# Performance work log

Hardware: AMD Instinct MI355X
Metric: run time of the kernel (lower is better)

Reference implementation:

```python
import jax, jax.numpy as jnp
import numpy as np

B, S, E, L, H, FF, CB = 16, 1000, 512, 4, 8, 2048, 4096
DH = E // H

def _ln(x, g, b):
    m = x.mean(-1, keepdims=True)
    v = ((x - m) ** 2).mean(-1, keepdims=True)
    return (x - m) / jnp.sqrt(v + 1e-5) * g + b

def setup_inputs() -> dict:
    key = jax.random.key(0)
    cnt = [0]
    def rn(shape, s=0.02):
        cnt[0] += 1
        return jax.random.normal(jax.random.fold_in(key, cnt[0]), shape, jnp.float32) * s
    inp = {}
    inp['noisy_tokens'] = jax.random.randint(jax.random.fold_in(key, 999), (B, S), 0, CB, dtype=jnp.int32)
    inp['codebook'] = rn((CB, E), 1.0)
    # sinusoidal positional encoding, as in _create_positional_encoding
    pe = np.zeros((S, E), np.float32)
    pos = np.arange(S, dtype=np.float32)[:, None]
    div = np.exp(np.arange(0, E, 2, dtype=np.float32) * (-np.log(10000.0) / E))
    pe[:, 0::2] = np.sin(pos * div)
    pe[:, 1::2] = np.cos(pos * div)
    inp['pos_enc'] = jnp.asarray(pe)[None]  # [1,S,E]
    # transformer encoder layers (stacked over L)
    inp['qkv_w'] = rn((L, 3 * E, E)); inp['qkv_b'] = jnp.zeros((L, 3 * E))
    inp['out_w'] = rn((L, E, E));     inp['out_b'] = jnp.zeros((L, E))
    inp['ln1_g'] = jnp.ones((L, E));  inp['ln1_b'] = jnp.zeros((L, E))
    inp['ln2_g'] = jnp.ones((L, E));  inp['ln2_b'] = jnp.zeros((L, E))
    inp['ff1_w'] = rn((L, FF, E));    inp['ff1_b'] = jnp.zeros((L, FF))
    inp['ff2_w'] = rn((L, E, FF));    inp['ff2_b'] = jnp.zeros((L, E))
    inp['fin_g'] = jnp.ones((E,));    inp['fin_b'] = jnp.zeros((E,))
    # post_process: Linear, LN, GELU, Linear
    inp['pp1_w'] = rn((E, E)); inp['pp1_b'] = jnp.zeros((E,))
    inp['pp_ln_g'] = jnp.ones((E,)); inp['pp_ln_b'] = jnp.zeros((E,))
    inp['pp2_w'] = rn((E, E)); inp['pp2_b'] = jnp.zeros((E,))
    inp['res_w'] = jnp.float32(0.1)
    # feature_to_codebook: Linear, LN, GELU, Linear (codebook_dim == E)
    inp['fc1_w'] = rn((E, E)); inp['fc1_b'] = jnp.zeros((E,))
    inp['fc_ln_g'] = jnp.ones((E,)); inp['fc_ln_b'] = jnp.zeros((E,))
    inp['fc2_w'] = rn((E, E)); inp['fc2_b'] = jnp.zeros((E,))
    return inp

def reference(noisy_tokens, codebook, pos_enc, qkv_w, qkv_b, out_w, out_b,
              ln1_g, ln1_b, ln2_g, ln2_b, ff1_w, ff1_b, ff2_w, ff2_b,
              fin_g, fin_b, pp1_w, pp1_b, pp_ln_g, pp_ln_b, pp2_w, pp2_b,
              res_w, fc1_w, fc1_b, fc_ln_g, fc_ln_b, fc2_w, fc2_b):
    gelu = lambda z: jax.nn.gelu(z, approximate=False)
    # token embedding (codebook_projection is Identity) + positional encoding
    x = codebook[noisy_tokens] + pos_enc            # [B,S,E]
    # pre-norm transformer encoder (dropout=0 / eval)
    y = x
    for l in range(L):
        h = _ln(y, ln1_g[l], ln1_b[l])
        qkv = h @ qkv_w[l].T + qkv_b[l]             # [B,S,3E]
        q, k, v = jnp.split(qkv, 3, axis=-1)
        q = q.reshape(B, S, H, DH); k = k.reshape(B, S, H, DH); v = v.reshape(B, S, H, DH)
        scores = jnp.einsum('bqhd,bkhd->bhqk', q, k) / jnp.sqrt(jnp.float32(DH))
        attn = jax.nn.softmax(scores, axis=-1)
        ctx = jnp.einsum('bhqk,bkhd->bqhd', attn, v).reshape(B, S, E)
        y = y + (ctx @ out_w[l].T + out_b[l])
        h2 = _ln(y, ln2_g[l], ln2_b[l])
        y = y + (gelu(h2 @ ff1_w[l].T + ff1_b[l]) @ ff2_w[l].T + ff2_b[l])
    y = _ln(y, fin_g, fin_b)
    # post_process + residual
    pp = gelu(_ln(y @ pp1_w.T + pp1_b, pp_ln_g, pp_ln_b)) @ pp2_w.T + pp2_b
    enhanced = x + res_w * pp
    # feature_to_codebook
    fc = gelu(_ln(enhanced @ fc1_w.T + fc1_b, fc_ln_g, fc_ln_b)) @ fc2_w.T + fc2_b  # [B,S,E]
    # quantize: nearest neighbour in codebook (cdist + argmin)
    flat = fc.reshape(-1, E)
    d2 = (jnp.sum(flat ** 2, -1, keepdims=True)
          - 2.0 * flat @ codebook.T
          + jnp.sum(codebook ** 2, -1))            # [B*S, CB]
    tokens = jnp.argmin(d2, axis=-1).reshape(B, S)
    return fc, tokens
```

## Files before the change

kernel.cpp:

```cpp
#include <hip/hip_runtime.h>
#include <hip/hip_bf16.h>
#include <math.h>

#define NTOK 16000
#define E    512
#define FFD  2048
#define CBN  4096
#define SEQ  1000
#define NH   8
#define VLD  1008

typedef __hip_bfloat16 bf16;
typedef __attribute__((ext_vector_type(8))) short short8;
typedef __attribute__((ext_vector_type(4))) float f32x4;

__device__ __forceinline__ float gelu_f(float v) {
    return 0.5f * v * (1.0f + erff(v * 0.70710678118654752f));
}

__device__ __forceinline__ void split_store(float v, bf16* hi, bf16* lo, size_t idx) {
    bf16 h = __float2bfloat16(v);
    hi[idx] = h;
    lo[idx] = __float2bfloat16(v - __bfloat162float(h));
}

__device__ __forceinline__ void gll16(const bf16* g, short* l) {
    __builtin_amdgcn_global_load_lds((const __attribute__((address_space(1))) void*)g,
                                     (__attribute__((address_space(3))) void*)l, 16, 0, 0);
}

__device__ __forceinline__ void t2_ins(float v, int c, float& v1, int& c1, float& v2, int& c2) {
    const bool b1 = (v < v1) || (v == v1 && c < c1);
    const bool b2 = (v < v2) || (v == v2 && c < c2);
    if (b1) { v2 = v1; c2 = c1; v1 = v; c1 = c; }
    else if (b2) { v2 = v; c2 = c; }
}

__global__ __launch_bounds__(128) void embed_kernel(const int* __restrict__ tok,
                                                    const float* __restrict__ cb,
                                                    const float* __restrict__ pe,
                                                    float* __restrict__ y) {
    const int row = blockIdx.x;
    const int s = row % SEQ;
    const int t = tok[row];
    const int c = threadIdx.x * 4;
    const float4 cv = *(const float4*)(cb + (size_t)t * E + c);
    const float4 pv = *(const float4*)(pe + (size_t)s * E + c);
    *(float4*)(y + (size_t)row * E + c) =
        make_float4(cv.x + pv.x, cv.y + pv.y, cv.z + pv.z, cv.w + pv.w);
}

__global__ __launch_bounds__(256) void split_w(const float* __restrict__ src, int ld,
                                               int cols_log2, int n,
                                               bf16* __restrict__ hi, bf16* __restrict__ lo) {
    const int i = blockIdx.x * 256 + threadIdx.x;
    if (i >= n) return;
    const int r = i >> cols_log2;
    const int c = i & ((1 << cols_log2) - 1);
    const float v = src[(size_t)r * ld + c];
    split_store(v, hi, lo, i);
}

template<int GELU>
__global__ __launch_bounds__(256) void ln_planes(const float* __restrict__ in,
                                                 bf16* __restrict__ hi, bf16* __restrict__ lo,
                                                 const float* __restrict__ g,
                                                 const float* __restrict__ b) {
    const int lane = threadIdx.x & 63;
    const int row = blockIdx.x * 4 + (threadIdx.x >> 6);
    const float* p = in + (size_t)row * E;
    const float4 v0 = *(const float4*)(p + lane * 4);
    const float4 v1 = *(const float4*)(p + 256 + lane * 4);
    float sum = v0.x + v0.y + v0.z + v0.w + v1.x + v1.y + v1.z + v1.w;
    float sq = v0.x * v0.x + v0.y * v0.y + v0.z * v0.z + v0.w * v0.w
             + v1.x * v1.x + v1.y * v1.y + v1.z * v1.z + v1.w * v1.w;
#pragma unroll
    for (int m = 1; m < 64; m <<= 1) {
        sum += __shfl_xor(sum, m);
        sq += __shfl_xor(sq, m);
    }
    const float mean = sum * (1.0f / 512.0f);
    const float var = sq * (1.0f / 512.0f) - mean * mean;
    const float rstd = rsqrtf(var + 1e-5f);
    const float4 g0 = *(const float4*)(g + lane * 4);
    const float4 g1 = *(const float4*)(g + 256 + lane * 4);
    const float4 b0 = *(const float4*)(b + lane * 4);
    const float4 b1 = *(const float4*)(b + 256 + lane * 4);
    const size_t base = (size_t)row * E;
    float o;
    const float vv0[4] = {v0.x, v0.y, v0.z, v0.w};
    const float gg0[4] = {g0.x, g0.y, g0.z, g0.w};
    const float bb0[4] = {b0.x, b0.y, b0.z, b0.w};
    const float vv1[4] = {v1.x, v1.y, v1.z, v1.w};
    const float gg1[4] = {g1.x, g1.y, g1.z, g1.w};
    const float bb1[4] = {b1.x, b1.y, b1.z, b1.w};
#pragma unroll
    for (int t = 0; t < 4; ++t) {
        o = (vv0[t] - mean) * rstd * gg0[t] + bb0[t];
        if (GELU) o = gelu_f(o);
        split_store(o, hi, lo, base + lane * 4 + t);
        o = (vv1[t] - mean) * rstd * gg1[t] + bb1[t];
        if (GELU) o = gelu_f(o);
        split_store(o, hi, lo, base + 256 + lane * 4 + t);
    }
}

template<int OUT>
__global__ __launch_bounds__(256) void gemm_split(
    const bf16* __restrict__ Ah, const bf16* __restrict__ Al, int lda,
    const bf16* __restrict__ Wh, const bf16* __restrict__ Wl, int ldw,
    const float* __restrict__ bias,
    float* __restrict__ C, int ldc,
    bf16* __restrict__ Ohi, bf16* __restrict__ Olo, int ldp,
    const int* __restrict__ noisy, const float* __restrict__ cb,
    const float* __restrict__ pe, const float* __restrict__ resw,
    int K) {
    __shared__ __align__(16) short SB[2][4][128][32];
    const int tid = threadIdx.x;
    const int rowBase = blockIdx.y * 128;
    const int colBase = blockIdx.x * 128;
    const int wave = tid >> 6, lane = tid & 63;
    const int wm = (wave & 1) * 64, wn = (wave >> 1) * 64;
    const int lm = lane & 15;
    const int psl8 = ((lane >> 4) ^ ((lm >> 1) & 3)) * 8;

    const bf16* src = (wave == 0) ? Ah : (wave == 1) ? Al : (wave == 2) ? Wh : Wl;
    const int sld = (wave < 2) ? lda : ldw;
    const int srb = (wave < 2) ? rowBase : colBase;
    const int sslot = (lane & 3) ^ ((lane >> 3) & 3);
    const bf16* sp = src + (size_t)(srb + (lane >> 2)) * sld + sslot * 8;
    short* lb0 = &SB[0][wave][0][0];
    short* lb1 = &SB[1][wave][0][0];

    f32x4 acc[4][4];
#pragma unroll
    for (int i = 0; i < 4; ++i)
#pragma unroll
        for (int j = 0; j < 4; ++j)
            acc[i][j] = (f32x4){0.f, 0.f, 0.f, 0.f};

    const int nt = K >> 5;
#pragma unroll
    for (int j = 0; j < 8; ++j)
        gll16(sp + (size_t)j * 16 * sld, lb0 + j * 512);
    {
        const bf16* p = sp + 32;
#pragma unroll
        for (int j = 0; j < 8; ++j)
            gll16(p + (size_t)j * 16 * sld, lb1 + j * 512);
    }
    for (int t = 0; t < nt; ++t) {
        const int cur = t & 1;
        if (t + 1 < nt) asm volatile("s_waitcnt vmcnt(8)" ::: "memory");
        else            asm volatile("s_waitcnt vmcnt(0)" ::: "memory");
        __builtin_amdgcn_s_barrier();
        __builtin_amdgcn_sched_barrier(0);
        const short (*P)[128][32] = SB[cur];
        short8 ah[4], al[4], wh[4], wl[4];
#pragma unroll
        for (int i = 0; i < 4; ++i) {
            ah[i] = *(const short8*)&P[0][wm + i * 16 + lm][psl8];
            al[i] = *(const short8*)&P[1][wm + i * 16 + lm][psl8];
            wh[i] = *(const short8*)&P[2][wn + i * 16 + lm][psl8];
            wl[i] = *(const short8*)&P[3][wn + i * 16 + lm][psl8];
        }
#pragma unroll
        for (int i = 0; i < 4; ++i)
#pragma unroll
            for (int j = 0; j < 4; ++j)
                acc[i][j] = __builtin_amdgcn_mfma_f32_16x16x32_bf16(ah[i], wh[j], acc[i][j], 0, 0, 0);
#pragma unroll
        for (int i = 0; i < 4; ++i)
#pragma unroll
            for (int j = 0; j < 4; ++j)
                acc[i][j] = __builtin_amdgcn_mfma_f32_16x16x32_bf16(ah[i], wl[j], acc[i][j], 0, 0, 0);
#pragma unroll
        for (int i = 0; i < 4; ++i)
#pragma unroll
            for (int j = 0; j < 4; ++j)
                acc[i][j] = __builtin_amdgcn_mfma_f32_16x16x32_bf16(al[i], wh[j], acc[i][j], 0, 0, 0);
        __builtin_amdgcn_s_barrier();
        if (t + 2 < nt) {
            short* lb = cur ? lb1 : lb0;
            const bf16* p = sp + (t + 2) * 32;
#pragma unroll
            for (int j = 0; j < 8; ++j)
                gll16(p + (size_t)j * 16 * sld, lb + j * 512);
        }
    }

    float bv[4];
#pragma unroll
    for (int j = 0; j < 4; ++j)
        bv[j] = bias ? bias[colBase + wn + j * 16 + lm] : 0.f;
    float scv = 0.f;
    if (OUT == 3) scv = resw[0];
#pragma unroll
    for (int i = 0; i < 4; ++i) {
#pragma unroll
        for (int reg = 0; reg < 4; ++reg) {
            const int r = rowBase + wm + i * 16 + (lane >> 4) * 4 + reg;
            int tok = 0, srow = 0;
            if (OUT == 3) { tok = noisy[r]; srow = r % SEQ; }
#pragma unroll
            for (int j = 0; j < 4; ++j) {
                const int col = colBase + wn + j * 16 + lm;
                float v = acc[i][j][reg] + bv[j];
                if (OUT == 0) {
                    C[(size_t)r * ldc + col] = v;
                } else if (OUT == 1) {
                    float* cp = C + (size_t)r * ldc + col;
                    *cp = *cp + v;
                } else if (OUT == 2) {
                    v = gelu_f(v);
                    split_store(v, Ohi, Olo, (size_t)r * ldp + col);
                } else if (OUT == 3) {
                    const float xv = cb[(size_t)tok * E + col] + pe[(size_t)srow * E + col];
                    v = xv + scv * v;
                    split_store(v, Ohi, Olo, (size_t)r * ldp + col);
                } else if (OUT == 4) {
                    split_store(v, Ohi, Olo, (size_t)r * ldp + col);
                } else {
                    C[(size_t)r * ldc + col] = v;
                    split_store(v, Ohi, Olo, (size_t)r * ldp + col);
                }
            }
        }
    }
}

__global__ __launch_bounds__(256) void vtrans(const bf16* __restrict__ vh_src,
                                              const bf16* __restrict__ vl_src,
                                              bf16* __restrict__ vth,
                                              bf16* __restrict__ vtl) {
    __shared__ short T[64][72];
    const int tid = threadIdx.x;
    const int st = blockIdx.x;
    const int bh = blockIdx.y;
    const int b = bh >> 3, h = bh & 7;
    const int sr = tid >> 2, dq = (tid & 3) * 16;
    const int s_g = st * 64 + sr;
    const int od = tid >> 3;
    const int osq = (tid & 7) * 8;
#pragma unroll
    for (int p = 0; p < 2; ++p) {
        const short* src = (const short*)(p ? vl_src : vh_src);
        short* dst = (short*)(p ? vtl : vth);
        short8 a0 = {0, 0, 0, 0, 0, 0, 0, 0};
        short8 a1 = {0, 0, 0, 0, 0, 0, 0, 0};
        if (s_g < SEQ) {
            const short* sp = src + (size_t)(b * SEQ + s_g) * 1536 + 1024 + h * 64 + dq;
            a0 = *(const short8*)sp;
            a1 = *(const short8*)(sp + 8);
        }
        __syncthreads();
#pragma unroll
        for (int j = 0; j < 8; ++j) T[dq + j][sr] = a0[j];
#pragma unroll
        for (int j = 0; j < 8; ++j) T[dq + 8 + j][sr] = a1[j];
        __syncthreads();
        const int scol = st * 64 + osq;
        if (scol + 8 <= VLD) {
            const short8 o0 = *(const short8*)&T[od][osq];
            const short8 o1 = *(const short8*)&T[od + 32][osq];
            *(short8*)(dst + (size_t)(bh * 64 + od) * VLD + scol) = o0;
            *(short8*)(dst + (size_t)(bh * 64 + od + 32) * VLD + scol) = o1;
        }
    }
}

__global__ __launch_bounds__(256) void attn_mfma(const bf16* __restrict__ qkh,
                                                 const bf16* __restrict__ qkl,
                                                 const bf16* __restrict__ vth,
                                                 const bf16* __restrict__ vtl,
                                                 bf16* __restrict__ chi,
                                                 bf16* __restrict__ clo) {
    __shared__ short QPs[2][64][72];
    __shared__ short Ks[2][64][72];
    __shared__ short Vs[2][64][72];
    const int tid = threadIdx.x;
    const int qt = blockIdx.x, bh = blockIdx.y;
    const int b = bh >> 3, h = bh & 7;
    const int wave = tid >> 6, lane = tid & 63;
    const int lm = lane & 15, g = lane >> 4, q8 = g * 8;
    const int wq = wave * 16;
    const int r0 = tid >> 2, kq = (tid & 3) * 16;
    const short8 z = {0, 0, 0, 0, 0, 0, 0, 0};

    {
        const int q = qt * 64 + r0;
        short8 a0 = z, a1 = z, b0 = z, b1 = z;
        if (q < SEQ) {
            const size_t base = (size_t)(b * SEQ + q) * 1536 + h * 64 + kq;
            a0 = *(const short8*)((const short*)qkh + base);
            a1 = *(const short8*)((const short*)qkh + base + 8);
            b0 = *(const short8*)((const short*)qkl + base);
            b1 = *(const short8*)((const short*)qkl + base + 8);
        }
        *(short8*)&QPs[0][r0][kq] = a0; *(short8*)&QPs[0][r0][kq + 8] = a1;
        *(short8*)&QPs[1][r0][kq] = b0; *(short8*)&QPs[1][r0][kq + 8] = b1;
    }
    __syncthreads();
    short8 qfh[2], qfl[2];
#pragma unroll
    for (int t = 0; t < 2; ++t) {
        qfh[t] = *(const short8*)&QPs[0][wq + lm][t * 32 + q8];
        qfl[t] = *(const short8*)&QPs[1][wq + lm][t * 32 + q8];
    }

    float m_i[4] = {-3e38f, -3e38f, -3e38f, -3e38f};
    float l_i[4] = {0.f, 0.f, 0.f, 0.f};
    f32x4 o[4];
#pragma unroll
    for (int dt = 0; dt < 4; ++dt) o[dt] = (f32x4){0.f, 0.f, 0.f, 0.f};

    short8 ka0 = z, ka1 = z, kl0 = z, kl1 = z;
    short8 va0 = z, va1 = z, vl0 = z, vl1 = z;
    auto loadKV = [&](int kb2) {
        const int kr = kb2 + r0;
        ka0 = z; ka1 = z; kl0 = z; kl1 = z;
        if (kr < SEQ) {
            const size_t base = (size_t)(b * SEQ + kr) * 1536 + 512 + h * 64 + kq;
            ka0 = *(const short8*)((const short*)qkh + base);
            ka1 = *(const short8*)((const short*)qkh + base + 8);
            kl0 = *(const short8*)((const short*)qkl + base);
            kl1 = *(const short8*)((const short*)qkl + base + 8);
        }
        const size_t vbase = (size_t)(bh * 64 + r0) * VLD + kb2 + kq;
        va0 = z; va1 = z; vl0 = z; vl1 = z;
        if (kb2 + kq + 8 <= VLD) {
            va0 = *(const short8*)((const short*)vth + vbase);
            vl0 = *(const short8*)((const short*)vtl + vbase);
        }
        if (kb2 + kq + 16 <= VLD) {
            va1 = *(const short8*)((const short*)vth + vbase + 8);
            vl1 = *(const short8*)((const short*)vtl + vbase + 8);
        }
    };
    loadKV(0);

    for (int kb = 0; kb < SEQ; kb += 64) {
        __syncthreads();
        {
            *(short8*)&Ks[0][r0][kq] = ka0; *(short8*)&Ks[0][r0][kq + 8] = ka1;
            *(short8*)&Ks[1][r0][kq] = kl0; *(short8*)&Ks[1][r0][kq + 8] = kl1;
            *(short8*)&Vs[0][r0][kq] = va0; *(short8*)&Vs[0][r0][kq + 8] = va1;
            *(short8*)&Vs[1][r0][kq] = vl0; *(short8*)&Vs[1][r0][kq + 8] = vl1;
        }
        __syncthreads();
        if (kb + 64 < SEQ) loadKV(kb + 64);
        f32x4 sac[4];
#pragma unroll
        for (int j = 0; j < 4; ++j) sac[j] = (f32x4){0.f, 0.f, 0.f, 0.f};
#pragma unroll
        for (int t = 0; t < 2; ++t) {
#pragma unroll
            for (int j = 0; j < 4; ++j) {
                const short8 kh = *(const short8*)&Ks[0][j * 16 + lm][t * 32 + q8];
                const short8 kl = *(const short8*)&Ks[1][j * 16 + lm][t * 32 + q8];
                sac[j] = __builtin_amdgcn_mfma_f32_16x16x32_bf16(qfh[t], kh, sac[j], 0, 0, 0);
                sac[j] = __builtin_amdgcn_mfma_f32_16x16x32_bf16(qfh[t], kl, sac[j], 0, 0, 0);
                sac[j] = __builtin_amdgcn_mfma_f32_16x16x32_bf16(qfl[t], kh, sac[j], 0, 0, 0);
            }
        }
        float alpha_v[4];
#pragma unroll
        for (int reg = 0; reg < 4; ++reg) {
            float sv[4];
            float rm = -3e38f;
#pragma unroll
            for (int j = 0; j < 4; ++j) {
                const int kc = kb + j * 16 + lm;
                float s = sac[j][reg] * 0.125f;
                s = (kc < SEQ) ? s : -3e38f;
                sv[j] = s;
                rm = fmaxf(rm, s);
            }
#pragma unroll
            for (int m = 1; m < 16; m <<= 1) rm = fmaxf(rm, __shfl_xor(rm, m));
            const float mn = fmaxf(m_i[reg], rm);
            const float al = expf(m_i[reg] - mn);
            float rs = 0.f;
            const int prow = wq + g * 4 + reg;
#pragma unroll
            for (int j = 0; j < 4; ++j) {
                const float pv = expf(sv[j] - mn);
                rs += pv;
                bf16 phb = __float2bfloat16(pv);
                bf16 plb = __float2bfloat16(pv - __bfloat162float(phb));
                QPs[0][prow][j * 16 + lm] = *reinterpret_cast<short*>(&phb);
                QPs[1][prow][j * 16 + lm] = *reinterpret_cast<short*>(&plb);
            }
#pragma unroll
            for (int m = 1; m < 16; m <<= 1) rs += __shfl_xor(rs, m);
            l_i[reg] = l_i[reg] * al + rs;
            m_i[reg] = mn;
            alpha_v[reg] = al;
        }
        const f32x4 av = {alpha_v[0], alpha_v[1], alpha_v[2], alpha_v[3]};
#pragma unroll
        for (int dt = 0; dt < 4; ++dt) o[dt] *= av;
        __syncthreads();
#pragma unroll
        for (int t = 0; t < 2; ++t) {
            const short8 ph = *(const short8*)&QPs[0][wq + lm][t * 32 + q8];
            const short8 pl = *(const short8*)&QPs[1][wq + lm][t * 32 + q8];
#pragma unroll
            for (int dt = 0; dt < 4; ++dt) {
                const short8 vh = *(const short8*)&Vs[0][dt * 16 + lm][t * 32 + q8];
                const short8 vl = *(const short8*)&Vs[1][dt * 16 + lm][t * 32 + q8];
                o[dt] = __builtin_amdgcn_mfma_f32_16x16x32_bf16(ph, vh, o[dt], 0, 0, 0);
                o[dt] = __builtin_amdgcn_mfma_f32_16x16x32_bf16(ph, vl, o[dt], 0, 0, 0);
                o[dt] = __builtin_amdgcn_mfma_f32_16x16x32_bf16(pl, vh, o[dt], 0, 0, 0);
            }
        }
    }
#pragma unroll
    for (int reg = 0; reg < 4; ++reg) {
        const int q = qt * 64 + wq + g * 4 + reg;
        if (q < SEQ) {
            const float inv = 1.0f / l_i[reg];
#pragma unroll
            for (int dt = 0; dt < 4; ++dt) {
                const size_t idx = (size_t)(b * SEQ + q) * E + h * 64 + dt * 16 + lm;
                split_store(o[dt][reg] * inv, chi, clo, idx);
            }
        }
    }
}

__global__ __launch_bounds__(256) void cbnorm_kernel(const float* __restrict__ cb,
                                                     float* __restrict__ out) {
    const int lane = threadIdx.x & 63;
    const int row = blockIdx.x * 4 + (threadIdx.x >> 6);
    const float* p = cb + (size_t)row * E;
    const float4 v0 = *(const float4*)(p + lane * 4);
    const float4 v1 = *(const float4*)(p + 256 + lane * 4);
    float sq = v0.x * v0.x + v0.y * v0.y + v0.z * v0.z + v0.w * v0.w
             + v1.x * v1.x + v1.y * v1.y + v1.z * v1.z + v1.w * v1.w;
#pragma unroll
    for (int m = 1; m < 64; m <<= 1) sq += __shfl_xor(sq, m);
    if (lane == 0) out[row] = sq;
}

__global__ __launch_bounds__(256, 1) void argmin_mfma(
    const bf16* __restrict__ Ah, const bf16* __restrict__ Al,
    const bf16* __restrict__ Wh, const bf16* __restrict__ Wl,
    const float* __restrict__ cbn, float4* __restrict__ part) {
    __shared__ __align__(16) short Wreg[2][8192];
    const int tid = threadIdx.x;
    const int rowBase = blockIdx.x * 64;
    const int wave = tid >> 6, lane = tid & 63;
    const int lm = lane & 15, g = lane >> 4;
    const int g8 = g * 8;
    const int psl8 = (g ^ ((lm >> 1) & 3)) * 8;
    const int sslot = (lane & 3) ^ ((lane >> 3) & 3);
    const int srow = lane >> 2;
    const int row = rowBase + wave * 16 + lm;

    short8 a_h[16], a_l[16];
#pragma unroll
    for (int c = 0; c < 16; ++c) {
        a_h[c] = *(const short8*)(Ah + (size_t)row * E + c * 32 + g8);
        a_l[c] = *(const short8*)(Al + (size_t)row * E + c * 32 + g8);
    }

    auto stageW = [&](int s) {
        const int ct = s >> 4, k = s & 15;
        const int colB = ct * 128;
        short* dstb = &Wreg[s & 1][0];
#pragma unroll
        for (int e = 0; e < 4; ++e) {
            const int m = wave * 4 + e;
            const int p = m >> 3;
            const int j = m & 7;
            const bf16* srcp = p ? Wl : Wh;
            gll16(srcp + (size_t)(colB + j * 16 + srow) * E + k * 32 + sslot * 8,
                  dstb + ((p * 128 + j * 16) * 32));
        }
    };
    stageW(0);
    stageW(1);

    float rv1[4], rv2[4];
    int rc1[4], rc2[4];
#pragma unroll
    for (int r = 0; r < 4; ++r) {
        rv1[r] = 3e38f; rv2[r] = 3e38f;
        rc1[r] = 0x7fffffff; rc2[r] = 0x7fffffff;
    }
    f32x4 acc[8];
#pragma unroll
    for (int j = 0; j < 8; ++j) acc[j] = (f32x4){0.f, 0.f, 0.f, 0.f};

    for (int ct = 0; ct < 32; ++ct) {
        const int colB = ct * 128;
#pragma unroll
        for (int k = 0; k < 16; ++k) {
            const int s = ct * 16 + k;
            if (s + 1 < 512) asm volatile("s_waitcnt vmcnt(4)" ::: "memory");
            else             asm volatile("s_waitcnt vmcnt(0)" ::: "memory");
            __builtin_amdgcn_s_barrier();
            __builtin_amdgcn_sched_barrier(0);
            const short* B = &Wreg[s & 1][0];
#pragma unroll
            for (int j = 0; j < 8; ++j) {
                const short8 wh = *(const short8*)(B + (j * 16 + lm) * 32 + psl8);
                const short8 wl = *(const short8*)(B + (128 + j * 16 + lm) * 32 + psl8);
                acc[j] = __builtin_amdgcn_mfma_f32_16x16x32_bf16(a_h[k], wh, acc[j], 0, 0, 0);
                acc[j] = __builtin_amdgcn_mfma_f32_16x16x32_bf16(a_h[k], wl, acc[j], 0, 0, 0);
                acc[j] = __builtin_amdgcn_mfma_f32_16x16x32_bf16(a_l[k], wh, acc[j], 0, 0, 0);
            }
            __builtin_amdgcn_s_barrier();
            if (s + 2 < 512) stageW(s + 2);
        }
#pragma unroll
        for (int j = 0; j < 8; ++j) {
            const int col = colB + j * 16 + lm;
            const float nv = cbn[col];
#pragma unroll
            for (int r = 0; r < 4; ++r) {
                const float d = nv - 2.0f * acc[j][r];
                t2_ins(d, col, rv1[r], rc1[r], rv2[r], rc2[r]);
            }
            acc[j] = (f32x4){0.f, 0.f, 0.f, 0.f};
        }
    }

#pragma unroll
    for (int r = 0; r < 4; ++r) {
#pragma unroll
        for (int m = 1; m < 16; m <<= 1) {
            const float w1 = __shfl_xor(rv1[r], m); const int d1 = __shfl_xor(rc1[r], m);
            const float w2 = __shfl_xor(rv2[r], m); const int d2 = __shfl_xor(rc2[r], m);
            t2_ins(w1, d1, rv1[r], rc1[r], rv2[r], rc2[r]);
            t2_ins(w2, d2, rv1[r], rc1[r], rv2[r], rc2[r]);
        }
    }
    if (lm == 0) {
#pragma unroll
        for (int r = 0; r < 4; ++r)
            part[rowBase + wave * 16 + g * 4 + r] =
                make_float4(rv1[r], (float)rc1[r], rv2[r], (float)rc2[r]);
    }
}

__global__ __launch_bounds__(256) void argmin_exact(const float4* __restrict__ part,
                                                    const float* __restrict__ fc,
                                                    const float* __restrict__ cb,
                                                    const float* __restrict__ cbn,
                                                    float* __restrict__ tokf) {
    const int wave = threadIdx.x >> 6, lane = threadIdx.x & 63;
    const int r = blockIdx.x * 4 + wave;
    const float4 p = part[r];
    const int c1 = (int)p.y;
    const int c2 = (int)p.w;
    const float* fr = fc + (size_t)r * E + lane * 8;
    const float* p1 = cb + (size_t)c1 * E + lane * 8;
    const float* p2 = cb + (size_t)c2 * E + lane * 8;
    float d1 = 0.f, d2 = 0.f;
#pragma unroll
    for (int j = 0; j < 8; ++j) {
        const float f = fr[j];
        d1 += f * p1[j];
        d2 += f * p2[j];
    }
#pragma unroll
    for (int m = 1; m < 64; m <<= 1) {
        d1 += __shfl_xor(d1, m);
        d2 += __shfl_xor(d2, m);
    }
    d1 = cbn[c1] - 2.0f * d1;
    d2 = cbn[c2] - 2.0f * d2;
    const int win = ((d1 < d2) || (d1 == d2 && c1 < c2)) ? c1 : c2;
    if (lane == 0) tokf[r] = (float)win;
}

extern "C" void kernel_launch(void* const* d_in, const int* in_sizes, int n_in,
                              void* d_out, int out_size, void* d_ws, size_t ws_size,
                              hipStream_t stream) {
    const int* noisy = (const int*)d_in[0];
    const float* codebook = (const float*)d_in[1];
    const float* pos_enc = (const float*)d_in[2];
    const float* qkv_w = (const float*)d_in[3];
    const float* qkv_b = (const float*)d_in[4];
    const float* out_w = (const float*)d_in[5];
    const float* out_b = (const float*)d_in[6];
    const float* ln1_g = (const float*)d_in[7];
    const float* ln1_b = (const float*)d_in[8];
    const float* ln2_g = (const float*)d_in[9];
    const float* ln2_b = (const float*)d_in[10];
    const float* ff1_w = (const float*)d_in[11];
    const float* ff1_b = (const float*)d_in[12];
    const float* ff2_w = (const float*)d_in[13];
    const float* ff2_b = (const float*)d_in[14];
    const float* fin_g = (const float*)d_in[15];
    const float* fin_b = (const float*)d_in[16];
    const float* pp1_w = (const float*)d_in[17];
    const float* pp1_b = (const float*)d_in[18];
    const float* pp_ln_g = (const float*)d_in[19];
    const float* pp_ln_b = (const float*)d_in[20];
    const float* pp2_w = (const float*)d_in[21];
    const float* pp2_b = (const float*)d_in[22];
    const float* res_w = (const float*)d_in[23];
    const float* fc1_w = (const float*)d_in[24];
    const float* fc1_b = (const float*)d_in[25];
    const float* fc_ln_g = (const float*)d_in[26];
    const float* fc_ln_b = (const float*)d_in[27];
    const float* fc2_w = (const float*)d_in[28];
    const float* fc2_b = (const float*)d_in[29];

    float* ws = (float*)d_ws;
    float* y = ws;
    float* REG = ws + 8192000;
    bf16* qkvh = (bf16*)REG;
    bf16* qkvl = qkvh + 24576000;
    bf16* mid_hi = (bf16*)REG;
    bf16* mid_lo = mid_hi + 16384000;
    float* slotA = REG;
    float* slotB = REG + 8192000;
    bf16* e_hi = (bf16*)slotA;
    bf16* e_lo = e_hi + 8192000;
    bf16* fcp2_hi = (bf16*)(REG + 16384000);
    bf16* fcp2_lo = fcp2_hi + 8192000;
    float* WV = ws + 32768000;
    bf16* vth = (bf16*)WV;
    bf16* vtl = vth + 8192 * VLD;
    bf16* wA_hi = (bf16*)WV;
    bf16* wA_lo = wA_hi + 1048576;
    bf16* wB_hi = wA_lo + 1048576;
    bf16* wB_lo = wB_hi + 1048576;
    bf16* cbh = wB_lo + 1048576;
    bf16* cbl = cbh + 2097152;
    float* cbn = slotB;
    float4* part = (float4*)(slotB + 4096);
    bf16* h_hi = (bf16*)d_out;
    bf16* h_lo = h_hi + 8192000;
    float* tokf = (float*)d_out + 8192000;

    const dim3 blk(256);
    const dim3 g512(4, 125), g1024(8, 125), g1536(12, 125);

    embed_kernel<<<dim3(NTOK), dim3(128), 0, stream>>>(noisy, codebook, pos_enc, y);

    for (int l = 0; l < 4; ++l) {
        ln_planes<0><<<dim3(4000), blk, 0, stream>>>(y, h_hi, h_lo, ln1_g + l * E, ln1_b + l * E);
        split_w<<<dim3(3072), blk, 0, stream>>>(qkv_w + (size_t)l * 1536 * E, E, 9, 1536 * E, wA_hi, wA_lo);
        gemm_split<4><<<g1536, blk, 0, stream>>>(
            h_hi, h_lo, E, wA_hi, wA_lo, E, qkv_b + (size_t)l * 1536,
            nullptr, 0, qkvh, qkvl, 1536, nullptr, nullptr, nullptr, nullptr, E);
        vtrans<<<dim3(16, 128), blk, 0, stream>>>(qkvh, qkvl, vth, vtl);
        attn_mfma<<<dim3(16, 128), blk, 0, stream>>>(qkvh, qkvl, vth, vtl, h_hi, h_lo);
        split_w<<<dim3(1024), blk, 0, stream>>>(out_w + (size_t)l * E * E, E, 9, E * E, wB_hi, wB_lo);
        gemm_split<1><<<g512, blk, 0, stream>>>(
            h_hi, h_lo, E, wB_hi, wB_lo, E, out_b + (size_t)l * E,
            y, E, nullptr, nullptr, 0, nullptr, nullptr, nullptr, nullptr, E);
        ln_planes<0><<<dim3(4000), blk, 0, stream>>>(y, h_hi, h_lo, ln2_g + l * E, ln2_b + l * E);
        split_w<<<dim3(4096), blk, 0, stream>>>(ff1_w + (size_t)l * FFD * E, E, 9, FFD * E, wA_hi, wA_lo);
        split_w<<<dim3(4096), blk, 0, stream>>>(ff2_w + (size_t)l * E * FFD, FFD, 11, E * FFD, wB_hi, wB_lo);
        for (int c = 0; c < 2; ++c) {
            gemm_split<2><<<g1024, blk, 0, stream>>>(
                h_hi, h_lo, E, wA_hi + (size_t)c * 1024 * E, wA_lo + (size_t)c * 1024 * E, E,
                ff1_b + (size_t)l * FFD + c * 1024,
                nullptr, 0, mid_hi, mid_lo, 1024, nullptr, nullptr, nullptr, nullptr, E);
            gemm_split<1><<<g512, blk, 0, stream>>>(
                mid_hi, mid_lo, 1024, wB_hi + c * 1024, wB_lo + c * 1024, FFD,
                (c == 0) ? (ff2_b + (size_t)l * E) : nullptr,
                y, E, nullptr, nullptr, 0, nullptr, nullptr, nullptr, nullptr, 1024);
        }
    }

    ln_planes<0><<<dim3(4000), blk, 0, stream>>>(y, h_hi, h_lo, fin_g, fin_b);
    split_w<<<dim3(1024), blk, 0, stream>>>(pp1_w, E, 9, E * E, wA_hi, wA_lo);
    gemm_split<0><<<g512, blk, 0, stream>>>(
        h_hi, h_lo, E, wA_hi, wA_lo, E, pp1_b,
        slotB, E, nullptr, nullptr, 0, nullptr, nullptr, nullptr, nullptr, E);
    ln_planes<1><<<dim3(4000), blk, 0, stream>>>(slotB, h_hi, h_lo, pp_ln_g, pp_ln_b);
    split_w<<<dim3(1024), blk, 0, stream>>>(pp2_w, E, 9, E * E, wB_hi, wB_lo);
    gemm_split<3><<<g512, blk, 0, stream>>>(
        h_hi, h_lo, E, wB_hi, wB_lo, E, pp2_b,
        nullptr, 0, e_hi, e_lo, E, noisy, codebook, pos_enc, res_w, E);
    split_w<<<dim3(1024), blk, 0, stream>>>(fc1_w, E, 9, E * E, wA_hi, wA_lo);
    gemm_split<0><<<g512, blk, 0, stream>>>(
        e_hi, e_lo, E, wA_hi, wA_lo, E, fc1_b,
        slotB, E, nullptr, nullptr, 0, nullptr, nullptr, nullptr, nullptr, E);
    ln_planes<1><<<dim3(4000), blk, 0, stream>>>(slotB, h_hi, h_lo, fc_ln_g, fc_ln_b);
    split_w<<<dim3(1024), blk, 0, stream>>>(fc2_w, E, 9, E * E, wB_hi, wB_lo);
    gemm_split<5><<<g512, blk, 0, stream>>>(
        h_hi, h_lo, E, wB_hi, wB_lo, E, fc2_b,
        slotA, E, fcp2_hi, fcp2_lo, E, nullptr, nullptr, nullptr, nullptr, E);

    split_w<<<dim3(8192), blk, 0, stream>>>(codebook, E, 9, CBN * E, cbh, cbl);
    cbnorm_kernel<<<dim3(1024), blk, 0, stream>>>(codebook, cbn);
    argmin_mfma<<<dim3(250), blk, 0, stream>>>(fcp2_hi, fcp2_lo, cbh, cbl, cbn, part);
    argmin_exact<<<dim3(4000), blk, 0, stream>>>(part, slotA, codebook, cbn, tokf);
    hipMemcpyAsync(d_out, slotA, (size_t)8192000 * 4, hipMemcpyDeviceToDevice, stream);
}
```

Measured before the change: 3.663 ms.

## Split argmin codebook columns across two wave groups with 512-thread blocks

Doubles the argmin_mfma block to 8 waves. Each row group of 16 rows is now handled by two waves, each covering half of the 128 codebook columns per tile, and the W staging load is split across all 8 waves. The two partial top-2 results per row are merged through shared memory at the end. This is meant to raise wave occupancy and latency hiding in the codebook distance kernel, which runs only 250 blocks. In exchange, every A fragment is now loaded into registers by twice as many waves, and the kernel gains a final shared-memory merge with extra barriers.

```diff
diff --git a/kernel.cpp b/kernel.cpp
--- a/kernel.cpp
+++ b/kernel.cpp
@@ -443,7 +443,7 @@
     if (lane == 0) out[row] = sq;
 }
 
-__global__ __launch_bounds__(256, 1) void argmin_mfma(
+__global__ __launch_bounds__(512) void argmin_mfma(
     const bf16* __restrict__ Ah, const bf16* __restrict__ Al,
     const bf16* __restrict__ Wh, const bf16* __restrict__ Wl,
     const float* __restrict__ cbn, float4* __restrict__ part) {
@@ -451,18 +451,25 @@
     const int tid = threadIdx.x;
     const int rowBase = blockIdx.x * 64;
     const int wave = tid >> 6, lane = tid & 63;
+    const int rowg = wave & 3;
+    const int chalf = wave >> 2;
     const int lm = lane & 15, g = lane >> 4;
     const int g8 = g * 8;
     const int psl8 = (g ^ ((lm >> 1) & 3)) * 8;
     const int sslot = (lane & 3) ^ ((lane >> 3) & 3);
     const int srow = lane >> 2;
-    const int row = rowBase + wave * 16 + lm;
+    const int row = rowBase + rowg * 16 + lm;
 
     short8 a_h[16], a_l[16];
 #pragma unroll
     for (int c = 0; c < 16; ++c) {
         a_h[c] = *(const short8*)(Ah + (size_t)row * E + c * 32 + g8);
         a_l[c] = *(const short8*)(Al + (size_t)row * E + c * 32 + g8);
+    }
+#pragma unroll
+    for (int c = 0; c < 16; ++c) {
+        asm volatile("" : "+v"(a_h[c]));
+        asm volatile("" : "+v"(a_l[c]));
     }
 
     auto stageW = [&](int s) {
@@ -470,8 +477,8 @@
         const int colB = ct * 128;
         short* dstb = &Wreg[s & 1][0];
 #pragma unroll
-        for (int e = 0; e < 4; ++e) {
-            const int m = wave * 4 + e;
+        for (int e = 0; e < 2; ++e) {
+            const int m = wave * 2 + e;
             const int p = m >> 3;
             const int j = m & 7;
             const bf16* srcp = p ? Wl : Wh;
@@ -489,24 +496,25 @@
         rv1[r] = 3e38f; rv2[r] = 3e38f;
         rc1[r] = 0x7fffffff; rc2[r] = 0x7fffffff;
     }
-    f32x4 acc[8];
-#pragma unroll
-    for (int j = 0; j < 8; ++j) acc[j] = (f32x4){0.f, 0.f, 0.f, 0.f};
+    f32x4 acc[4];
+#pragma unroll
+    for (int j = 0; j < 4; ++j) acc[j] = (f32x4){0.f, 0.f, 0.f, 0.f};
 
     for (int ct = 0; ct < 32; ++ct) {
         const int colB = ct * 128;
 #pragma unroll
         for (int k = 0; k < 16; ++k) {
             const int s = ct * 16 + k;
-            if (s + 1 < 512) asm volatile("s_waitcnt vmcnt(4)" ::: "memory");
+            if (s + 1 < 512) asm volatile("s_waitcnt vmcnt(2)" ::: "memory");
             else             asm volatile("s_waitcnt vmcnt(0)" ::: "memory");
             __builtin_amdgcn_s_barrier();
             __builtin_amdgcn_sched_barrier(0);
             const short* B = &Wreg[s & 1][0];
 #pragma unroll
-            for (int j = 0; j < 8; ++j) {
-                const short8 wh = *(const short8*)(B + (j * 16 + lm) * 32 + psl8);
-                const short8 wl = *(const short8*)(B + (128 + j * 16 + lm) * 32 + psl8);
+            for (int j = 0; j < 4; ++j) {
+                const int jj = chalf * 4 + j;
+                const short8 wh = *(const short8*)(B + (jj * 16 + lm) * 32 + psl8);
+                const short8 wl = *(const short8*)(B + (128 + jj * 16 + lm) * 32 + psl8);
                 acc[j] = __builtin_amdgcn_mfma_f32_16x16x32_bf16(a_h[k], wh, acc[j], 0, 0, 0);
                 acc[j] = __builtin_amdgcn_mfma_f32_16x16x32_bf16(a_h[k], wl, acc[j], 0, 0, 0);
                 acc[j] = __builtin_amdgcn_mfma_f32_16x16x32_bf16(a_l[k], wh, acc[j], 0, 0, 0);
@@ -515,8 +523,8 @@
             if (s + 2 < 512) stageW(s + 2);
         }
 #pragma unroll
-        for (int j = 0; j < 8; ++j) {
-            const int col = colB + j * 16 + lm;
+        for (int j = 0; j < 4; ++j) {
+            const int col = colB + (chalf * 4 + j) * 16 + lm;
             const float nv = cbn[col];
 #pragma unroll
             for (int r = 0; r < 4; ++r) {
@@ -537,11 +545,23 @@
             t2_ins(w2, d2, rv1[r], rc1[r], rv2[r], rc2[r]);
         }
     }
+    __syncthreads();
+    float4* mbuf = reinterpret_cast<float4*>(&Wreg[0][0]);
     if (lm == 0) {
 #pragma unroll
         for (int r = 0; r < 4; ++r)
-            part[rowBase + wave * 16 + g * 4 + r] =
+            mbuf[(rowg * 16 + g * 4 + r) * 2 + chalf] =
                 make_float4(rv1[r], (float)rc1[r], rv2[r], (float)rc2[r]);
+    }
+    __syncthreads();
+    if (tid < 64) {
+        const float4 p0 = mbuf[tid * 2 + 0];
+        const float4 p1 = mbuf[tid * 2 + 1];
+        float v1 = p0.x, v2 = p0.z;
+        int c1 = (int)p0.y, c2 = (int)p0.w;
+        t2_ins(p1.x, (int)p1.y, v1, c1, v2, c2);
+        t2_ins(p1.z, (int)p1.w, v1, c1, v2, c2);
+        part[rowBase + tid] = make_float4(v1, (float)c1, v2, (float)c2);
     }
 }
 
@@ -692,7 +712,7 @@
 
     split_w<<<dim3(8192), blk, 0, stream>>>(codebook, E, 9, CBN * E, cbh, cbl);
     cbnorm_kernel<<<dim3(1024), blk, 0, stream>>>(codebook, cbn);
-    argmin_mfma<<<dim3(250), blk, 0, stream>>>(fcp2_hi, fcp2_lo, cbh, cbl, cbn, part);
+    argmin_mfma<<<dim3(250), dim3(512), 0, stream>>>(fcp2_hi, fcp2_lo, cbh, cbl, cbn, part);
     argmin_exact<<<dim3(4000), blk, 0, stream>>>(part, slotA, codebook, cbn, tokf);
     hipMemcpyAsync(d_out, slotA, (size_t)8192000 * 4, hipMemcpyDeviceToDevice, stream);
 }
```

After: 3.549 ms. 1.03x faster.
